# Performance work log

Hardware: AMD Instinct MI355X
Metric: run time of the kernel (lower is better)

Reference implementation:

```python
import jax, jax.numpy as jnp
import numpy as np

S, B, H, L = 1024, 128, 1024, 2
D = 2 * H  # concat dim: hidden + input (input_size == hidden_size)


def setup_inputs() -> dict:
    key = jax.random.key(0)
    k1, k2, k3 = jax.random.split(key, 3)
    inputs = jax.random.normal(k1, (S, B, H), dtype=jnp.float32)
    lim = 1.0 / np.sqrt(D)  # torch Linear default init range
    W = jax.random.uniform(k2, (L, 4, D), jnp.float32, -lim, lim)  # rows: i, c~, f, o
    b = jax.random.uniform(k3, (L, 4), jnp.float32, -lim, lim)
    return {"inputs": inputs, "W": W, "b": b}


def _lstm(inputs, W, b):
    Ln = W.shape[0]
    Bn, Hd = inputs.shape[1], inputs.shape[2]
    h0 = jnp.zeros((Ln, Bn, Hd), inputs.dtype)
    c0 = jnp.zeros_like(h0)

    def step(carry, x_t):
        h, c = carry  # each [L, B, H]
        inp = x_t     # [B, H]
        hs, cs = [], []
        for l in range(Ln):
            z = jnp.concatenate([h[l], inp], axis=-1)  # [B, 2H], order [H_t_1, X_t]
            g = z @ W[l].T + b[l]                       # [B, 4] — four 1-out Linears fused
            i_t = jax.nn.sigmoid(g[:, 0:1])
            c_hat = jnp.tanh(g[:, 1:2])
            f_t = jax.nn.sigmoid(g[:, 2:3])
            o_t = jax.nn.sigmoid(g[:, 3:4])
            c_new = f_t * c[l] + i_t * c_hat            # scalar gates broadcast over [B, H]
            h_new = o_t * jnp.tanh(c_new)
            hs.append(h_new)
            cs.append(c_new)
            inp = h_new
        h = jnp.stack(hs)
        c = jnp.stack(cs)
        return (h, c), h[-1]

    (hT, cT), outs = jax.lax.scan(step, (h0, c0), inputs)
    return outs, hT, cT  # outs: [S, B, H]


def reference(inputs, W, b):
    outs, hT, cT = _lstm(inputs, W, b)
    return (outs, (hT, cT))
```

## Files before the change

### kernel.cpp

```cpp
#include <hip/hip_runtime.h>

#define SS 1024
#define BB 128
#define HH 1024
#define LL 2
#define DD 2048
#define NROWS (SS*BB)
#define TSEG 256
#define NSEG 4
#define ROWSEG (TSEG*BB)
#define RPW 4
#define NSCANB 16
#define NWORKB 2048
#define L2E  1.4426950408889634f

typedef float f32x4 __attribute__((ext_vector_type(4)));

__device__ __forceinline__ float fast_rcp(float x)  { return __builtin_amdgcn_rcpf(x); }
__device__ __forceinline__ float exp2_(float x)     { return __builtin_amdgcn_exp2f(x); }

template<int CTRL>
__device__ __forceinline__ float qperm(float x){
    return __int_as_float(__builtin_amdgcn_update_dpp(0, __float_as_int(x), CTRL, 0xF, 0xF, true));
}
__device__ __forceinline__ float rowshr4(float x){
    return __int_as_float(__builtin_amdgcn_update_dpp(0, __float_as_int(x), 0x114, 0xF, 0xF, true));
}

__global__ __launch_bounds__(256) void fused_phase(
    const float* __restrict__ x, const float* __restrict__ W,
    const float* __restrict__ bias, float* out,
    float* __restrict__ s_out, float* __restrict__ finals,
    float* __restrict__ sums, float* __restrict__ state,
    int s1, int s2, int s3, int fin)
{
    float* pre = out + (size_t)NROWS * HH;
    const int tid = threadIdx.x;

    if (blockIdx.x < NSCANB) {
        if (tid >= 64) return;
        const int lane = tid;

        if (s2 < 0) {
            if (blockIdx.x == 0 && s1 == 0) {
                for (int s = 0; s < 12; ++s) {
                    const int base = (s < 4) ? s*DD
                                   : (s < 8) ? 4*DD + (s-4)*DD
                                             : 4*DD + (s-8)*DD + HH;
                    float v = 0.f;
                    #pragma unroll
                    for (int k = 0; k < 16; ++k) v += W[base + lane + k*64];
                    #pragma unroll
                    for (int off = 32; off >= 1; off >>= 1) v += __shfl_xor(v, off, 64);
                    if (lane == 0) sums[s] = v;
                }
            }
            return;
        }

        const int gate = lane & 3;
        const int L    = (lane >> 2) & 1;
        const int lb   = lane >> 3;
        const int bb   = blockIdx.x * 8 + lb;

        const float sh = sums[L*4 + gate];
        const float sx = sums[8 + gate];
        const float sc  = (gate == 1) ? (2.0f*L2E) : (-L2E);
        const float s_h = sh * sc;
        const float sxc = L ? sx * sc : 0.0f;
        const float pcc = L ? bias[4+gate] * sc : 0.0f;
        const float Ac  = (gate == 1) ? 1.0f : 0.0f;
        const float Bc  = (gate == 0) ? (2.0f*L2E) : ((gate == 1) ? -2.0f : 1.0f);

        const float* pbase = pre + ((size_t)bb << 12) + gate;
        float* obase = s_out + bb;

        const int t_lo = s2 * TSEG, t_hi = t_lo + TSEG;

        float h, cp, h0d1, h0d2;
        float4* st = (float4*)state + blockIdx.x*64 + lane;
        if (t_lo == 0) { h = 0.f; cp = 0.f; h0d1 = 0.f; h0d2 = 0.f; }
        else { float4 s = *st; h = s.x; cp = s.y; h0d1 = s.z; h0d2 = s.w; }

        constexpr int PF = 16;
        float buf[PF];
        #pragma unroll
        for (int u = 0; u < PF; ++u) buf[u] = pbase[(size_t)(t_lo + u) * 4];

        for (int t0 = t_lo; t0 < t_hi; t0 += PF) {
            #pragma unroll
            for (int u = 0; u < PF; ++u) {
                const int t = t0 + u;
                const float p = L ? pcc : buf[u];
                int tn = t + PF; if (tn > t_hi-1) tn = t_hi-1;
                buf[u] = pbase[(size_t)tn * 4];

                const float P = fmaf(h0d2, sxc, p);
                const float g = fmaf(h, s_h, P);
                const float v = fmaf(Bc, fast_rcp(1.0f + exp2_(g)), Ac);
                const float w = v * qperm<0xB1>(v);
                const float cpn = fmaf(qperm<0xAA>(v), cp, qperm<0x00>(w));
                const float th = fmaf(-2.0f, fast_rcp(1.0f + exp2_(cpn)), 1.0f);
                const float hn = qperm<0xFF>(v) * th;
                const bool disc = (u < 2) && (t0 == t_lo) && L;
                h  = disc ? h  : hn;
                cp = disc ? cp : cpn;
                h0d2 = h0d1;
                h0d1 = rowshr4(h);
                if (L && t >= t_lo + 2) obase[(size_t)(t-2) * BB] = h;
            }
        }

        const float h0f = h, c0f = cp;

        #pragma unroll
        for (int fs = 0; fs < 2; ++fs) {
            const float p = L ? pcc : buf[0];
            const float P = fmaf(h0d2, sxc, p);
            const float g = fmaf(h, s_h, P);
            const float v = fmaf(Bc, fast_rcp(1.0f + exp2_(g)), Ac);
            const float w = v * qperm<0xB1>(v);
            const float cpn = fmaf(qperm<0xAA>(v), cp, qperm<0x00>(w));
            const float th = fmaf(-2.0f, fast_rcp(1.0f + exp2_(cpn)), 1.0f);
            const float hn = qperm<0xFF>(v) * th;
            if (L) { h = hn; cp = cpn; obase[(size_t)(t_hi-2+fs) * BB] = hn; }
            h0d2 = h0d1;
        }

        *st = make_float4(h, cp, h0d1, h0d2);

        if (t_hi == SS && gate == 0) {
            if (L) { finals[128+bb] = h;   finals[384+bb] = cp  * (0.5f/L2E); }
            else   { finals[bb]     = h0f; finals[256+bb] = c0f * (0.5f/L2E); }
        }
        return;
    }

    const int lane = tid & 63;
    const int gw   = (blockIdx.x - NSCANB)*4 + (tid >> 6);

    if (s1 >= 0) {
        float4 wv[4][4];
        #pragma unroll
        for (int j = 0; j < 4; ++j)
            #pragma unroll
            for (int it = 0; it < 4; ++it)
                wv[j][it] = *(const float4*)(W + j*DD + HH + it*256 + lane*4);
        const float4 b0 = *(const float4*)(bias);

        #pragma unroll 2
        for (int j = 0; j < RPW; ++j) {
            const int row = s1*ROWSEG + gw*RPW + j;
            const float* xr = x + (size_t)row * HH;
            float a0 = 0.f, a1 = 0.f, a2 = 0.f, a3 = 0.f;
            #pragma unroll
            for (int it = 0; it < 4; ++it) {
                f32x4 xv = __builtin_nontemporal_load((const f32x4*)xr + it*64 + lane);
                a0 = fmaf(xv.x, wv[0][it].x, fmaf(xv.y, wv[0][it].y, fmaf(xv.z, wv[0][it].z, fmaf(xv.w, wv[0][it].w, a0))));
                a1 = fmaf(xv.x, wv[1][it].x, fmaf(xv.y, wv[1][it].y, fmaf(xv.z, wv[1][it].z, fmaf(xv.w, wv[1][it].w, a1))));
                a2 = fmaf(xv.x, wv[2][it].x, fmaf(xv.y, wv[2][it].y, fmaf(xv.z, wv[2][it].z, fmaf(xv.w, wv[2][it].w, a2))));
                a3 = fmaf(xv.x, wv[3][it].x, fmaf(xv.y, wv[3][it].y, fmaf(xv.z, wv[3][it].z, fmaf(xv.w, wv[3][it].w, a3))));
            }
            #pragma unroll
            for (int off = 32; off >= 1; off >>= 1) {
                a0 += __shfl_xor(a0, off, 64);
                a1 += __shfl_xor(a1, off, 64);
                a2 += __shfl_xor(a2, off, 64);
                a3 += __shfl_xor(a3, off, 64);
            }
            if (lane == 0) {
                float4 r = make_float4((a0 + b0.x) * (-L2E),
                                       (a1 + b0.y) * ( 2.0f * L2E),
                                       (a2 + b0.z) * (-L2E),
                                       (a3 + b0.w) * (-L2E));
                const int b = row & (BB-1), t = row >> 7;
                *(float4*)(pre + (((size_t)b << 10) + t) * 4) = r;
            }
        }
    }

    if (s3 >= 0) {
        const int r0 = s3*ROWSEG + gw*RPW;
        const float4 v0 = *(const float4*)(s_out + r0);
        const float vs[RPW] = {v0.x, v0.y, v0.z, v0.w};
        #pragma unroll
        for (int j = 0; j < RPW; ++j) {
            const f32x4 vv = {vs[j], vs[j], vs[j], vs[j]};
            f32x4* dst = (f32x4*)(out + (size_t)(r0 + j) * HH);
            #pragma unroll
            for (int it = 0; it < 4; ++it)
                __builtin_nontemporal_store(vv, dst + it*64 + lane);
        }
    }

    if (fin && gw < 512) {
        const float v = finals[gw];
        const f32x4 vv = {v, v, v, v};
        f32x4* dst = (f32x4*)(out + (size_t)(NROWS + gw) * HH);
        #pragma unroll
        for (int it = 0; it < 4; ++it)
            __builtin_nontemporal_store(vv, dst + it*64 + lane);
    }
}

extern "C" void kernel_launch(void* const* d_in, const int* in_sizes, int n_in,
                              void* d_out, int out_size, void* d_ws, size_t ws_size,
                              hipStream_t stream) {
    const float* x    = (const float*)d_in[0];
    const float* W    = (const float*)d_in[1];
    const float* bias = (const float*)d_in[2];
    float* out = (float*)d_out;

    float* s_out  = (float*)d_ws;
    float* finals = s_out + NROWS;
    float* sums   = finals + 512;
    float* state  = sums + 16;

    for (int p = 0; p < NSEG + 2; ++p) {
        const int a1 = (p <= NSEG - 1) ? p : -1;
        const int a2 = (p >= 1 && p <= NSEG) ? p - 1 : -1;
        const int a3 = (p >= 2) ? p - 2 : -1;
        const int fn = (p == NSEG + 1) ? 1 : 0;
        hipLaunchKernelGGL(fused_phase, dim3(NSCANB + NWORKB), dim3(256), 0, stream,
                           x, W, bias, out, s_out, finals, sums, state,
                           a1, a2, a3, fn);
    }
}
```

Before: 236.0 us.

## Replace multi-launch phase pipeline with single persistent dataflow kernel using flags

Merges the six phase launches into one persistent kernel. Producer blocks compute input projections per segment and signal completion through atomic counters, scan waves spin-wait on those counters, and broadcast-writer blocks wait on scan flags. Segments are made finer (16 of 64 steps) so the three stages overlap more tightly. This removes launch and grid-wide barrier overhead, but it relies on all blocks being co-resident, and the guarded spin loops can silently give wrong results if the guard expires.

```diff
diff --git a/kernel.cpp b/kernel.cpp
--- a/kernel.cpp
+++ b/kernel.cpp
@@ -3,21 +3,34 @@
 #define SS 1024
 #define BB 128
 #define HH 1024
-#define LL 2
 #define DD 2048
 #define NROWS (SS*BB)
-#define TSEG 256
-#define NSEG 4
+#define NSEG 16
+#define TSEG 64
 #define ROWSEG (TSEG*BB)
-#define RPW 4
-#define NSCANB 16
-#define NWORKB 2048
+#define NSCANB 4
+#define NK1B   512
+#define NK3B   504
+#define NBLK   (NSCANB+NK1B+NK3B)
+#define K1WAVES 2048
 #define L2E  1.4426950408889634f
+#define PF 16
+
+#define K1FLAG(s,sh) (((s)*8 + (sh))*32)
+#define SCFLAG(s)    (4096 + (s)*32)
+#define FLAG_INTS    4608
 
 typedef float f32x4 __attribute__((ext_vector_type(4)));
 
 __device__ __forceinline__ float fast_rcp(float x)  { return __builtin_amdgcn_rcpf(x); }
 __device__ __forceinline__ float exp2_(float x)     { return __builtin_amdgcn_exp2f(x); }
+
+__device__ __forceinline__ void st_dev(float* p, float v){
+    __hip_atomic_store(p, v, __ATOMIC_RELAXED, __HIP_MEMORY_SCOPE_AGENT);
+}
+__device__ __forceinline__ float ld_dev(const float* p){
+    return __hip_atomic_load(p, __ATOMIC_RELAXED, __HIP_MEMORY_SCOPE_AGENT);
+}
 
 template<int CTRL>
 __device__ __forceinline__ float qperm(float x){
@@ -27,44 +40,38 @@
     return __int_as_float(__builtin_amdgcn_update_dpp(0, __float_as_int(x), 0x114, 0xF, 0xF, true));
 }
 
-__global__ __launch_bounds__(256) void fused_phase(
+__global__ __launch_bounds__(256, 4) void lstm_df(
     const float* __restrict__ x, const float* __restrict__ W,
     const float* __restrict__ bias, float* out,
     float* __restrict__ s_out, float* __restrict__ finals,
-    float* __restrict__ sums, float* __restrict__ state,
-    int s1, int s2, int s3, int fin)
+    int* __restrict__ flags)
 {
     float* pre = out + (size_t)NROWS * HH;
-    const int tid = threadIdx.x;
-
-    if (blockIdx.x < NSCANB) {
-        if (tid >= 64) return;
-        const int lane = tid;
-
-        if (s2 < 0) {
-            if (blockIdx.x == 0 && s1 == 0) {
-                for (int s = 0; s < 12; ++s) {
-                    const int base = (s < 4) ? s*DD
-                                   : (s < 8) ? 4*DD + (s-4)*DD
-                                             : 4*DD + (s-8)*DD + HH;
-                    float v = 0.f;
-                    #pragma unroll
-                    for (int k = 0; k < 16; ++k) v += W[base + lane + k*64];
-                    #pragma unroll
-                    for (int off = 32; off >= 1; off >>= 1) v += __shfl_xor(v, off, 64);
-                    if (lane == 0) sums[s] = v;
-                }
-            }
-            return;
-        }
-
+    const int tid  = threadIdx.x;
+    const int lane = tid & 63;
+    const int wv   = tid >> 6;
+    const int blk  = blockIdx.x;
+
+    if (blk < NSCANB) {
+        const int sw   = blk*4 + wv;
         const int gate = lane & 3;
         const int L    = (lane >> 2) & 1;
         const int lb   = lane >> 3;
-        const int bb   = blockIdx.x * 8 + lb;
-
-        const float sh = sums[L*4 + gate];
-        const float sx = sums[8 + gate];
+        const int bb   = sw*8 + lb;
+
+        float sh = 0.f, sx = 0.f;
+        for (int q = 0; q < 12; ++q) {
+            const int base = (q < 4) ? q*DD
+                           : (q < 8) ? 4*DD + (q-4)*DD
+                                     : 4*DD + (q-8)*DD + HH;
+            float v = 0.f;
+            #pragma unroll
+            for (int k = 0; k < 16; ++k) v += W[base + lane + k*64];
+            #pragma unroll
+            for (int off = 32; off >= 1; off >>= 1) v += __shfl_xor(v, off, 64);
+            if (q == L*4 + gate) sh = v;
+            if (q == 8 + gate)   sx = v;
+        }
         const float sc  = (gate == 1) ? (2.0f*L2E) : (-L2E);
         const float s_h = sh * sc;
         const float sxc = L ? sx * sc : 0.0f;
@@ -75,26 +82,58 @@
         const float* pbase = pre + ((size_t)bb << 12) + gate;
         float* obase = s_out + bb;
 
-        const int t_lo = s2 * TSEG, t_hi = t_lo + TSEG;
-
-        float h, cp, h0d1, h0d2;
-        float4* st = (float4*)state + blockIdx.x*64 + lane;
-        if (t_lo == 0) { h = 0.f; cp = 0.f; h0d1 = 0.f; h0d2 = 0.f; }
-        else { float4 s = *st; h = s.x; cp = s.y; h0d1 = s.z; h0d2 = s.w; }
-
-        constexpr int PF = 16;
-        float buf[PF];
-        #pragma unroll
-        for (int u = 0; u < PF; ++u) buf[u] = pbase[(size_t)(t_lo + u) * 4];
-
-        for (int t0 = t_lo; t0 < t_hi; t0 += PF) {
-            #pragma unroll
-            for (int u = 0; u < PF; ++u) {
-                const int t = t0 + u;
-                const float p = L ? pcc : buf[u];
-                int tn = t + PF; if (tn > t_hi-1) tn = t_hi-1;
-                buf[u] = pbase[(size_t)tn * 4];
-
+        float h = 0.f, cp = 0.f, h0d1 = 0.f, h0d2 = 0.f;
+
+        for (int s = 0; s < NSEG; ++s) {
+            {
+                int guard = 0;
+                for (;;) {
+                    int tot = 0;
+                    #pragma unroll
+                    for (int i = 0; i < 8; ++i)
+                        tot += __hip_atomic_load(&flags[K1FLAG(s,i)], __ATOMIC_RELAXED, __HIP_MEMORY_SCOPE_AGENT);
+                    if (tot >= K1WAVES) break;
+                    __builtin_amdgcn_s_sleep(8);
+                    if (++guard > (1<<20)) break;
+                }
+                asm volatile("" ::: "memory");
+            }
+            const int t_lo = s*TSEG, t_hi = t_lo + TSEG;
+            float buf[PF];
+            #pragma unroll
+            for (int u = 0; u < PF; ++u)
+                buf[u] = ld_dev(pbase + (size_t)(t_lo + u) * 4);
+
+            for (int t0 = t_lo; t0 < t_hi; t0 += PF) {
+                #pragma unroll
+                for (int u = 0; u < PF; ++u) {
+                    const int t = t0 + u;
+                    const float p = L ? pcc : buf[u];
+                    int tn = t + PF; if (tn > t_hi-1) tn = t_hi-1;
+                    buf[u] = ld_dev(pbase + (size_t)tn * 4);
+
+                    const float P = fmaf(h0d2, sxc, p);
+                    const float g = fmaf(h, s_h, P);
+                    const float v = fmaf(Bc, fast_rcp(1.0f + exp2_(g)), Ac);
+                    const float w = v * qperm<0xB1>(v);
+                    const float cpn = fmaf(qperm<0xAA>(v), cp, qperm<0x00>(w));
+                    const float th = fmaf(-2.0f, fast_rcp(1.0f + exp2_(cpn)), 1.0f);
+                    const float hn = qperm<0xFF>(v) * th;
+                    const bool disc = (u < 2) && (t0 == t_lo) && L;
+                    h  = disc ? h  : hn;
+                    cp = disc ? cp : cpn;
+                    h0d2 = h0d1;
+                    h0d1 = rowshr4(h);
+                    if (L && t >= t_lo + 2)
+                        st_dev(obase + (size_t)(t-2) * BB, h);
+                }
+            }
+
+            const float h0f = h, c0f = cp;
+
+            #pragma unroll
+            for (int fs = 0; fs < 2; ++fs) {
+                const float p = L ? pcc : buf[0];
                 const float P = fmaf(h0d2, sxc, p);
                 const float g = fmaf(h, s_h, P);
                 const float v = fmaf(Bc, fast_rcp(1.0f + exp2_(g)), Ac);
@@ -102,101 +141,105 @@
                 const float cpn = fmaf(qperm<0xAA>(v), cp, qperm<0x00>(w));
                 const float th = fmaf(-2.0f, fast_rcp(1.0f + exp2_(cpn)), 1.0f);
                 const float hn = qperm<0xFF>(v) * th;
-                const bool disc = (u < 2) && (t0 == t_lo) && L;
-                h  = disc ? h  : hn;
-                cp = disc ? cp : cpn;
+                if (L) { h = hn; cp = cpn;
+                         st_dev(obase + (size_t)(t_hi-2+fs) * BB, hn); }
                 h0d2 = h0d1;
-                h0d1 = rowshr4(h);
-                if (L && t >= t_lo + 2) obase[(size_t)(t-2) * BB] = h;
-            }
-        }
-
-        const float h0f = h, c0f = cp;
-
-        #pragma unroll
-        for (int fs = 0; fs < 2; ++fs) {
-            const float p = L ? pcc : buf[0];
-            const float P = fmaf(h0d2, sxc, p);
-            const float g = fmaf(h, s_h, P);
-            const float v = fmaf(Bc, fast_rcp(1.0f + exp2_(g)), Ac);
-            const float w = v * qperm<0xB1>(v);
-            const float cpn = fmaf(qperm<0xAA>(v), cp, qperm<0x00>(w));
-            const float th = fmaf(-2.0f, fast_rcp(1.0f + exp2_(cpn)), 1.0f);
-            const float hn = qperm<0xFF>(v) * th;
-            if (L) { h = hn; cp = cpn; obase[(size_t)(t_hi-2+fs) * BB] = hn; }
-            h0d2 = h0d1;
-        }
-
-        *st = make_float4(h, cp, h0d1, h0d2);
-
-        if (t_hi == SS && gate == 0) {
-            if (L) { finals[128+bb] = h;   finals[384+bb] = cp  * (0.5f/L2E); }
-            else   { finals[bb]     = h0f; finals[256+bb] = c0f * (0.5f/L2E); }
+            }
+
+            if (s == NSEG-1 && gate == 0) {
+                if (L) { st_dev(finals + 128 + bb, h);
+                         st_dev(finals + 384 + bb, cp  * (0.5f/L2E)); }
+                else   { st_dev(finals + bb,       h0f);
+                         st_dev(finals + 256 + bb, c0f * (0.5f/L2E)); }
+            }
+
+            __builtin_amdgcn_s_waitcnt(0);
+            if (lane == 0)
+                __hip_atomic_fetch_add(&flags[SCFLAG(s)], 1, __ATOMIC_RELAXED, __HIP_MEMORY_SCOPE_AGENT);
         }
         return;
     }
 
-    const int lane = tid & 63;
-    const int gw   = (blockIdx.x - NSCANB)*4 + (tid >> 6);
-
-    if (s1 >= 0) {
-        float4 wv[4][4];
+    if (blk < NSCANB + NK1B) {
+        const int i = (blk - NSCANB)*4 + wv;
+        float4 wvv[4][4];
         #pragma unroll
         for (int j = 0; j < 4; ++j)
             #pragma unroll
             for (int it = 0; it < 4; ++it)
-                wv[j][it] = *(const float4*)(W + j*DD + HH + it*256 + lane*4);
+                wvv[j][it] = *(const float4*)(W + j*DD + HH + it*256 + lane*4);
         const float4 b0 = *(const float4*)(bias);
 
-        #pragma unroll 2
-        for (int j = 0; j < RPW; ++j) {
-            const int row = s1*ROWSEG + gw*RPW + j;
-            const float* xr = x + (size_t)row * HH;
-            float a0 = 0.f, a1 = 0.f, a2 = 0.f, a3 = 0.f;
-            #pragma unroll
-            for (int it = 0; it < 4; ++it) {
-                f32x4 xv = __builtin_nontemporal_load((const f32x4*)xr + it*64 + lane);
-                a0 = fmaf(xv.x, wv[0][it].x, fmaf(xv.y, wv[0][it].y, fmaf(xv.z, wv[0][it].z, fmaf(xv.w, wv[0][it].w, a0))));
-                a1 = fmaf(xv.x, wv[1][it].x, fmaf(xv.y, wv[1][it].y, fmaf(xv.z, wv[1][it].z, fmaf(xv.w, wv[1][it].w, a1))));
-                a2 = fmaf(xv.x, wv[2][it].x, fmaf(xv.y, wv[2][it].y, fmaf(xv.z, wv[2][it].z, fmaf(xv.w, wv[2][it].w, a2))));
-                a3 = fmaf(xv.x, wv[3][it].x, fmaf(xv.y, wv[3][it].y, fmaf(xv.z, wv[3][it].z, fmaf(xv.w, wv[3][it].w, a3))));
-            }
-            #pragma unroll
-            for (int off = 32; off >= 1; off >>= 1) {
-                a0 += __shfl_xor(a0, off, 64);
-                a1 += __shfl_xor(a1, off, 64);
-                a2 += __shfl_xor(a2, off, 64);
-                a3 += __shfl_xor(a3, off, 64);
-            }
-            if (lane == 0) {
-                float4 r = make_float4((a0 + b0.x) * (-L2E),
-                                       (a1 + b0.y) * ( 2.0f * L2E),
-                                       (a2 + b0.z) * (-L2E),
-                                       (a3 + b0.w) * (-L2E));
-                const int b = row & (BB-1), t = row >> 7;
-                *(float4*)(pre + (((size_t)b << 10) + t) * 4) = r;
-            }
-        }
-    }
-
-    if (s3 >= 0) {
-        const int r0 = s3*ROWSEG + gw*RPW;
-        const float4 v0 = *(const float4*)(s_out + r0);
-        const float vs[RPW] = {v0.x, v0.y, v0.z, v0.w};
-        #pragma unroll
-        for (int j = 0; j < RPW; ++j) {
-            const f32x4 vv = {vs[j], vs[j], vs[j], vs[j]};
-            f32x4* dst = (f32x4*)(out + (size_t)(r0 + j) * HH);
-            #pragma unroll
-            for (int it = 0; it < 4; ++it)
-                __builtin_nontemporal_store(vv, dst + it*64 + lane);
-        }
-    }
-
-    if (fin && gw < 512) {
-        const float v = finals[gw];
+        for (int s = 0; s < NSEG; ++s) {
+            #pragma unroll 2
+            for (int j = 0; j < 4; ++j) {
+                const int row = s*ROWSEG + i*4 + j;
+                const float* xr = x + (size_t)row * HH;
+                float a0 = 0.f, a1 = 0.f, a2 = 0.f, a3 = 0.f;
+                #pragma unroll
+                for (int it = 0; it < 4; ++it) {
+                    f32x4 xv = __builtin_nontemporal_load((const f32x4*)xr + it*64 + lane);
+                    a0 = fmaf(xv.x, wvv[0][it].x, fmaf(xv.y, wvv[0][it].y, fmaf(xv.z, wvv[0][it].z, fmaf(xv.w, wvv[0][it].w, a0))));
+                    a1 = fmaf(xv.x, wvv[1][it].x, fmaf(xv.y, wvv[1][it].y, fmaf(xv.z, wvv[1][it].z, fmaf(xv.w, wvv[1][it].w, a1))));
+                    a2 = fmaf(xv.x, wvv[2][it].x, fmaf(xv.y, wvv[2][it].y, fmaf(xv.z, wvv[2][it].z, fmaf(xv.w, wvv[2][it].w, a2))));
+                    a3 = fmaf(xv.x, wvv[3][it].x, fmaf(xv.y, wvv[3][it].y, fmaf(xv.z, wvv[3][it].z, fmaf(xv.w, wvv[3][it].w, a3))));
+                }
+                #pragma unroll
+                for (int off = 32; off >= 1; off >>= 1) {
+                    a0 += __shfl_xor(a0, off, 64);
+                    a1 += __shfl_xor(a1, off, 64);
+                    a2 += __shfl_xor(a2, off, 64);
+                    a3 += __shfl_xor(a3, off, 64);
+                }
+                if (lane == 0) {
+                    const int b = row & (BB-1), t = row >> 7;
+                    float* pr = pre + (((size_t)b << 10) + t) * 4;
+                    st_dev(pr + 0, (a0 + b0.x) * (-L2E));
+                    st_dev(pr + 1, (a1 + b0.y) * ( 2.0f * L2E));
+                    st_dev(pr + 2, (a2 + b0.z) * (-L2E));
+                    st_dev(pr + 3, (a3 + b0.w) * (-L2E));
+                }
+            }
+            __builtin_amdgcn_s_waitcnt(0);
+            if (lane == 0)
+                __hip_atomic_fetch_add(&flags[K1FLAG(s, i & 7)], 1, __ATOMIC_RELAXED, __HIP_MEMORY_SCOPE_AGENT);
+        }
+        return;
+    }
+
+    const int u = (blk - NSCANB - NK1B)*4 + wv;
+    const int lbase = (u < 32) ? u*8 : 256 + (u-32)*4;
+    const int cnt   = (u < 32) ? 8 : 4;
+    for (int s = 0; s < NSEG; ++s) {
+        {
+            int guard = 0;
+            while (__hip_atomic_load(&flags[SCFLAG(s)], __ATOMIC_RELAXED, __HIP_MEMORY_SCOPE_AGENT) < 16) {
+                __builtin_amdgcn_s_sleep(32);
+                if (++guard > (1<<19)) break;
+            }
+            asm volatile("" ::: "memory");
+        }
+        const int r0 = s*ROWSEG + lbase;
+        for (int q = 0; q < cnt; q += 4) {
+            float vb0 = ld_dev(s_out + r0 + q + 0);
+            float vb1 = ld_dev(s_out + r0 + q + 1);
+            float vb2 = ld_dev(s_out + r0 + q + 2);
+            float vb3 = ld_dev(s_out + r0 + q + 3);
+            #pragma unroll
+            for (int jj = 0; jj < 4; ++jj) {
+                const float vb = (jj==0) ? vb0 : (jj==1) ? vb1 : (jj==2) ? vb2 : vb3;
+                const f32x4 vv = {vb, vb, vb, vb};
+                f32x4* dst = (f32x4*)(out + (size_t)(r0 + q + jj) * HH);
+                #pragma unroll
+                for (int it = 0; it < 4; ++it)
+                    __builtin_nontemporal_store(vv, dst + it*64 + lane);
+            }
+        }
+    }
+    if (u < 512) {
+        const float v = ld_dev(finals + u);
         const f32x4 vv = {v, v, v, v};
-        f32x4* dst = (f32x4*)(out + (size_t)(NROWS + gw) * HH);
+        f32x4* dst = (f32x4*)(out + (size_t)(NROWS + u) * HH);
         #pragma unroll
         for (int it = 0; it < 4; ++it)
             __builtin_nontemporal_store(vv, dst + it*64 + lane);
@@ -213,16 +256,9 @@
 
     float* s_out  = (float*)d_ws;
     float* finals = s_out + NROWS;
-    float* sums   = finals + 512;
-    float* state  = sums + 16;
-
-    for (int p = 0; p < NSEG + 2; ++p) {
-        const int a1 = (p <= NSEG - 1) ? p : -1;
-        const int a2 = (p >= 1 && p <= NSEG) ? p - 1 : -1;
-        const int a3 = (p >= 2) ? p - 2 : -1;
-        const int fn = (p == NSEG + 1) ? 1 : 0;
-        hipLaunchKernelGGL(fused_phase, dim3(NSCANB + NWORKB), dim3(256), 0, stream,
-                           x, W, bias, out, s_out, finals, sums, state,
-                           a1, a2, a3, fn);
-    }
-}
+    int*   flags  = (int*)(finals + 512);
+
+    hipMemsetAsync(flags, 0, FLAG_INTS * sizeof(int), stream);
+    hipLaunchKernelGGL(lstm_df, dim3(NBLK), dim3(256), 0, stream,
+                       x, W, bias, out, s_out, finals, flags);
+}
```

Result: slower. 336.0 us (+42.4%).
